# Kernel tuning notes

Hardware: AMD Instinct MI355X
Metric: run time of the kernel (lower is better)

Reference implementation:

```python
import jax, jax.numpy as jnp
import numpy as np

NUM_HEADS = 4
NUM_GROUPS = 32
EPS = 1e-6


def group_norm(x, gamma, beta):
    # x: [b, c, h, w]
    b, c, h, w = x.shape
    xg = x.reshape(b, NUM_GROUPS, c // NUM_GROUPS, h, w)
    mu = xg.mean(axis=(2, 3, 4), keepdims=True)
    var = xg.var(axis=(2, 3, 4), keepdims=True)
    xn = ((xg - mu) * jax.lax.rsqrt(var + EPS)).reshape(b, c, h, w)
    return xn * gamma[None, :, None, None] + beta[None, :, None, None]


def conv1x1(x, W, b):
    # 1x1 conv == per-pixel channel matmul. W: [out_c, in_c], b: [out_c]
    return jnp.einsum('bchw,oc->bohw', x, W) + b[None, :, None, None]


def setup_inputs() -> dict:
    key = jax.random.key(0)
    ks = jax.random.split(key, 8)
    c = 256
    b, h, w = 1, 64, 64
    s = 1.0 / np.sqrt(c)
    return {
        'x_kv': jax.random.normal(ks[0], (b, c, h, w), dtype=jnp.float32),
        'gn_gamma': jnp.ones((c,), dtype=jnp.float32),
        'gn_beta': jnp.zeros((c,), dtype=jnp.float32),
        'Wq': jax.random.normal(ks[1], (c, c), dtype=jnp.float32) * s,
        'bq': jnp.zeros((c,), dtype=jnp.float32),
        'Wk': jax.random.normal(ks[2], (c, c), dtype=jnp.float32) * s,
        'bk': jnp.zeros((c,), dtype=jnp.float32),
        'Wv': jax.random.normal(ks[3], (c, c), dtype=jnp.float32) * s,
        'bv': jnp.zeros((c,), dtype=jnp.float32),
        'Wp': jax.random.normal(ks[4], (c, c), dtype=jnp.float32) * s,
        'bp': jnp.zeros((c,), dtype=jnp.float32),
    }


def reference(x_kv, gn_gamma, gn_beta, Wq, bq, Wk, bk, Wv, bv, Wp, bp):
    b, c, h, w = x_kv.shape
    hd = c // NUM_HEADS
    n = h * w

    h_norm = group_norm(x_kv, gn_gamma, gn_beta)  # self-attn: same norm for q,k,v

    q = conv1x1(h_norm, Wq, bq).reshape(b, NUM_HEADS, hd, n).transpose(0, 1, 3, 2)  # [b,H,n,hd]
    k = conv1x1(h_norm, Wk, bk).reshape(b, NUM_HEADS, hd, n)                        # [b,H,hd,n]
    v = conv1x1(h_norm, Wv, bv).reshape(b, NUM_HEADS, hd, n).transpose(0, 1, 3, 2)  # [b,H,n,hd]

    scores = jnp.einsum('bhnd,bhdm->bhnm', q, k) * (hd ** -0.5)  # [b,H,n,n]
    attn = jax.nn.softmax(scores, axis=-1)
    out = jnp.einsum('bhnm,bhmd->bhnd', attn, v)  # [b,H,n,hd]

    # Faithful to torch: permute(0,2,1,3).contiguous().view(b,c,h,w)
    out = out.transpose(0, 2, 1, 3).reshape(b, c, h, w)
    return x_kv + conv1x1(out, Wp, bp)
```

## Files before the change

kernel.cpp:

```cpp
#include <hip/hip_runtime.h>
#include <hip/hip_bf16.h>

#define NPIX 4096
#define CCH  256
#define HD   64
#define GSIZE 32768

#define QSCALE 0.18033688f

typedef __bf16 bf16x8 __attribute__((ext_vector_type(8)));
typedef __bf16 bf16x4 __attribute__((ext_vector_type(4)));
typedef __bf16 bf16x2 __attribute__((ext_vector_type(2)));
typedef float  f32x4  __attribute__((ext_vector_type(4)));
typedef unsigned int uint32x4 __attribute__((ext_vector_type(4)));

#define XPITCH 264

#if __has_builtin(__builtin_amdgcn_exp2f)
#define EXP2(x) __builtin_amdgcn_exp2f(x)
#else
#define EXP2(x) __expf((x) * 0.6931471805599453f)
#endif


__device__ __forceinline__ unsigned pack_bf16x2(float lo, float hi)
{
    bf16x2 v;
    v[0] = (__bf16)lo;
    v[1] = (__bf16)hi;
    return __builtin_bit_cast(unsigned, v);
}

__global__ __launch_bounds__(256) void stats_wconv(
    const float* __restrict__ X,
    const float* __restrict__ Wq, const float* __restrict__ Wk,
    const float* __restrict__ Wv, const float* __restrict__ Wp,
    float* __restrict__ psum, float* __restrict__ pssq, __bf16* __restrict__ Wb)
{
    const int bid = blockIdx.x, t = threadIdx.x;
    if (bid < 256) {
        const float* base = X + bid * 4096;
        float sum = 0.f, ssq = 0.f;
        #pragma unroll
        for (int k = 0; k < 4; ++k) {
            float4 v = *(const float4*)(base + t * 4 + k * 1024);
            sum += v.x + v.y + v.z + v.w;
            ssq += v.x * v.x + v.y * v.y + v.z * v.z + v.w * v.w;
        }
        #pragma unroll
        for (int off = 1; off < 64; off <<= 1) {
            sum += __shfl_xor(sum, off);
            ssq += __shfl_xor(ssq, off);
        }
        __shared__ float red[2][4];
        const int wv = t >> 6;
        if ((t & 63) == 0) { red[0][wv] = sum; red[1][wv] = ssq; }
        __syncthreads();
        if (t == 0) {
            psum[bid] = red[0][0] + red[0][1] + red[0][2] + red[0][3];
            pssq[bid] = red[1][0] + red[1][1] + red[1][2] + red[1][3];
        }
    } else {
        const int j0 = (bid - 256) * 4096 + t * 16;
        const int m  = j0 >> 16;
        const float* W = (m == 0) ? Wq : (m == 1) ? Wk : (m == 2) ? Wv : Wp;
        const float sc = (m == 0) ? QSCALE : 1.f;
        const int off = j0 & 65535;
        #pragma unroll
        for (int k = 0; k < 4; ++k) {
            float4 v = *(const float4*)(W + off + k * 4);
            bf16x4 o;
            o[0] = (__bf16)(v.x * sc); o[1] = (__bf16)(v.y * sc);
            o[2] = (__bf16)(v.z * sc); o[3] = (__bf16)(v.w * sc);
            *(bf16x4*)(Wb + m * 65536 + off + k * 4) = o;
        }
    }
}

__global__ __launch_bounds__(256) void gn_qkv(
    const float* __restrict__ X, const float* __restrict__ gamma,
    const float* __restrict__ beta,
    const float* __restrict__ psum, const float* __restrict__ pssq,
    const __bf16* __restrict__ Wb,
    const float* __restrict__ bq, const float* __restrict__ bk,
    const float* __restrict__ bv,
    __bf16* __restrict__ Qb, __bf16* __restrict__ Kb, __bf16* __restrict__ Vb)
{
    __shared__ __bf16 tile[64 * XPITCH];
    __shared__ float al[256], bl[256];

    const int t = threadIdx.x, lane = t & 63, wave = t >> 6;
    const int l16 = lane & 15, quad = lane >> 4;
    const int p0 = blockIdx.x * 64;
    const int z = blockIdx.y >> 1, och = blockIdx.y & 1;

    {
        const int g = t >> 3;
        float s = 0.f, q = 0.f;
        #pragma unroll
        for (int j = 0; j < 8; ++j) { s += psum[g * 8 + j]; q += pssq[g * 8 + j]; }
        const float mu  = s * (1.f / GSIZE);
        const float var = q * (1.f / GSIZE) - mu * mu;
        const float a = gamma[t] * rsqrtf(var + 1e-6f);
        al[t] = a;
        bl[t] = beta[t] - mu * a;
    }
    __syncthreads();

    #pragma unroll 4
    for (int i = 0; i < 16; ++i) {
        const int c4 = wave * 64 + i * 4;
        f32x4 a4 = *(const f32x4*)(al + c4);
        f32x4 b4 = *(const f32x4*)(bl + c4);
        bf16x4 pk;
        pk[0] = (__bf16)(X[(c4 + 0) * NPIX + p0 + lane] * a4[0] + b4[0]);
        pk[1] = (__bf16)(X[(c4 + 1) * NPIX + p0 + lane] * a4[1] + b4[1]);
        pk[2] = (__bf16)(X[(c4 + 2) * NPIX + p0 + lane] * a4[2] + b4[2]);
        pk[3] = (__bf16)(X[(c4 + 3) * NPIX + p0 + lane] * a4[3] + b4[3]);
        *(bf16x4*)(tile + lane * XPITCH + c4) = pk;
    }
    __syncthreads();

    const int pw = wave * 16;
    bf16x8 xf[8];
    #pragma unroll
    for (int kc = 0; kc < 8; ++kc)
        xf[kc] = *(const bf16x8*)(tile + (pw + l16) * XPITCH + kc * 32 + quad * 8);

    const __bf16* Wz = Wb + z * 65536;
    const float* bias = (z == 0) ? bq : (z == 1) ? bk : bv;

    if (z < 2) {
        const float qs = (z == 0) ? QSCALE : 1.f;
        __bf16* dst = (z == 0) ? Qb : Kb;
        #pragma unroll
        for (int grp = 0; grp < 2; ++grp) {
            f32x4 acc[4] = {};
            #pragma unroll
            for (int kc = 0; kc < 8; ++kc) {
                #pragma unroll
                for (int u = 0; u < 4; ++u) {
                    bf16x8 wf = *(const bf16x8*)(Wz + (och * 128 + (grp * 4 + u) * 16 + l16) * CCH + kc * 32 + quad * 8);
                    acc[u] = __builtin_amdgcn_mfma_f32_16x16x32_bf16(wf, xf[kc], acc[u], 0, 0, 0);
                }
            }
            #pragma unroll
            for (int u = 0; u < 4; ++u) {
                const int ot = och * 8 + grp * 4 + u;
                f32x4 bz = *(const f32x4*)(bias + och * 128 + (grp * 4 + u) * 16 + quad * 4);
                bf16x4 o;
                o[0] = (__bf16)(acc[u][0] + bz[0] * qs);
                o[1] = (__bf16)(acc[u][1] + bz[1] * qs);
                o[2] = (__bf16)(acc[u][2] + bz[2] * qs);
                o[3] = (__bf16)(acc[u][3] + bz[3] * qs);
                const int head = ot >> 2, dloc = (ot & 3) * 16 + quad * 4;
                *(bf16x4*)(dst + head * (NPIX * HD) + (p0 + pw + l16) * HD + dloc) = o;
            }
        }
    } else {
        #pragma unroll
        for (int grp = 0; grp < 2; ++grp) {
            f32x4 acc[4] = {};
            #pragma unroll
            for (int kc = 0; kc < 8; ++kc) {
                #pragma unroll
                for (int u = 0; u < 4; ++u) {
                    bf16x8 wf = *(const bf16x8*)(Wz + (och * 128 + (grp * 4 + u) * 16 + l16) * CCH + kc * 32 + quad * 8);
                    acc[u] = __builtin_amdgcn_mfma_f32_16x16x32_bf16(xf[kc], wf, acc[u], 0, 0, 0);
                }
            }
            #pragma unroll
            for (int u = 0; u < 4; ++u) {
                const int oc = och * 128 + (grp * 4 + u) * 16 + l16;
                const float bz = bias[oc];
                bf16x4 o;
                o[0] = (__bf16)(acc[u][0] + bz); o[1] = (__bf16)(acc[u][1] + bz);
                o[2] = (__bf16)(acc[u][2] + bz); o[3] = (__bf16)(acc[u][3] + bz);
                *(bf16x4*)(Vb + oc * NPIX + p0 + pw + quad * 4) = o;
            }
        }
    }
}

__global__ __launch_bounds__(256, 1) void attn_mfma(
    const __bf16* __restrict__ Qb, const __bf16* __restrict__ Kb,
    const __bf16* __restrict__ Vb, __bf16* __restrict__ Sb)
{
    __shared__ __align__(16) float co[4 * 64 * 68];
    __shared__ float cl[4 * 64];

    const int t = threadIdx.x, lane = t & 63, wave = t >> 6;
    const int l16 = lane & 15, quad = lane >> 4;

    const int bid  = blockIdx.x;
    const int head = (bid & 7) >> 1;
    const int qt   = ((bid >> 3) << 1) | (bid & 1);
    const int p0   = qt * 64;

    const __bf16* Qh = Qb + head * (NPIX * HD);
    const __bf16* Kh = Kb + head * (NPIX * HD) + (wave * 32 + l16) * HD + quad * 8;
    const __bf16* Vh = Vb + head * (HD * NPIX) + l16 * NPIX + wave * 32 + quad * 8;

    bf16x8 qf[4][2];
    #pragma unroll
    for (int rt = 0; rt < 4; ++rt) {
        const __bf16* qp = Qh + (p0 + rt * 16 + l16) * HD + quad * 8;
        qf[rt][0] = *(const bf16x8*)(qp);
        qf[rt][1] = *(const bf16x8*)(qp + 32);
    }

    bf16x8 ones;
    #pragma unroll
    for (int j = 0; j < 8; ++j) ones[j] = (__bf16)1.0f;

    f32x4 l_acc[4] = {};
    f32x4 o_acc[4][4] = {};

    bf16x8 kA0, kA1, kA2, kA3, vA0, vA1, vA2, vA3;
    bf16x8 kB0, kB1, kB2, kB3, vB0, vB1, vB2, vB3;
    f32x4 sA0[4], sA1[4], sB0[4], sB1[4];
    bf16x8 bp[4];

    auto ldK = [&](int it, bf16x8& k0, bf16x8& k1, bf16x8& k2, bf16x8& k3) {
        const __bf16* kp = Kh + it * (128 * HD);
        k0 = *(const bf16x8*)(kp);
        k1 = *(const bf16x8*)(kp + 32);
        k2 = *(const bf16x8*)(kp + 16 * HD);
        k3 = *(const bf16x8*)(kp + 16 * HD + 32);
    };
    auto ldV = [&](int it, bf16x8& v0, bf16x8& v1, bf16x8& v2, bf16x8& v3) {
        const __bf16* vp = Vh + it * 128;
        v0 = *(const bf16x8*)(vp);
        v1 = *(const bf16x8*)(vp + 16 * NPIX);
        v2 = *(const bf16x8*)(vp + 32 * NPIX);
        v3 = *(const bf16x8*)(vp + 48 * NPIX);
    };
    auto qk = [&](bf16x8 k0, bf16x8 k1, bf16x8 k2, bf16x8 k3,
                  f32x4 (&s0)[4], f32x4 (&s1)[4]) {
        #pragma unroll
        for (int rt = 0; rt < 4; ++rt) {
            f32x4 z = {0.f, 0.f, 0.f, 0.f};
            s0[rt] = __builtin_amdgcn_mfma_f32_16x16x32_bf16(k0, qf[rt][0], z, 0, 0, 0);
            s0[rt] = __builtin_amdgcn_mfma_f32_16x16x32_bf16(k1, qf[rt][1], s0[rt], 0, 0, 0);
            s1[rt] = __builtin_amdgcn_mfma_f32_16x16x32_bf16(k2, qf[rt][0], z, 0, 0, 0);
            s1[rt] = __builtin_amdgcn_mfma_f32_16x16x32_bf16(k3, qf[rt][1], s1[rt], 0, 0, 0);
        }
    };
    auto exppack = [&](const f32x4 (&s0)[4], const f32x4 (&s1)[4]) {
        #pragma unroll
        for (int rt = 0; rt < 4; ++rt) {
            unsigned a0 = pack_bf16x2(EXP2(s0[rt][0]), EXP2(s0[rt][1]));
            unsigned a1 = pack_bf16x2(EXP2(s0[rt][2]), EXP2(s0[rt][3]));
            unsigned b0 = pack_bf16x2(EXP2(s1[rt][0]), EXP2(s1[rt][1]));
            unsigned b1 = pack_bf16x2(EXP2(s1[rt][2]), EXP2(s1[rt][3]));
            asm("v_permlane32_swap_b32 %0, %1" : "+v"(a0), "+v"(b0));
            asm("v_permlane32_swap_b32 %0, %1" : "+v"(a1), "+v"(b1));
            asm("v_permlane16_swap_b32 %0, %1" : "+v"(a0), "+v"(b0));
            asm("v_permlane16_swap_b32 %0, %1" : "+v"(a1), "+v"(b1));
            uint32x4 w;
            w[0] = a0; w[1] = a1; w[2] = b0; w[3] = b1;
            bp[rt] = __builtin_bit_cast(bf16x8, w);
        }
    };
    auto pv = [&](bf16x8 v0, bf16x8 v1, bf16x8 v2, bf16x8 v3) {
        #pragma unroll
        for (int rt = 0; rt < 4; ++rt) {
            l_acc[rt] = __builtin_amdgcn_mfma_f32_16x16x32_bf16(ones, bp[rt], l_acc[rt], 0, 0, 0);
            o_acc[0][rt] = __builtin_amdgcn_mfma_f32_16x16x32_bf16(v0, bp[rt], o_acc[0][rt], 0, 0, 0);
            o_acc[1][rt] = __builtin_amdgcn_mfma_f32_16x16x32_bf16(v1, bp[rt], o_acc[1][rt], 0, 0, 0);
            o_acc[2][rt] = __builtin_amdgcn_mfma_f32_16x16x32_bf16(v2, bp[rt], o_acc[2][rt], 0, 0, 0);
            o_acc[3][rt] = __builtin_amdgcn_mfma_f32_16x16x32_bf16(v3, bp[rt], o_acc[3][rt], 0, 0, 0);
        }
    };

    ldK(0, kA0, kA1, kA2, kA3);  ldV(0, vA0, vA1, vA2, vA3);
    ldK(1, kB0, kB1, kB2, kB3);  ldV(1, vB0, vB1, vB2, vB3);
    qk(kA0, kA1, kA2, kA3, sA0, sA1);

    #pragma unroll 1
    for (int it = 0; it < 32; it += 2) {
        const int n2 = (it + 2 < 32) ? it + 2 : 31;
        const int n3 = (it + 3 < 32) ? it + 3 : 31;

        qk(kB0, kB1, kB2, kB3, sB0, sB1);
        ldK(n2, kA0, kA1, kA2, kA3);
        exppack(sA0, sA1);
        pv(vA0, vA1, vA2, vA3);
        ldV(n2, vA0, vA1, vA2, vA3);
        exppack(sB0, sB1);
        qk(kA0, kA1, kA2, kA3, sA0, sA1);
        pv(vB0, vB1, vB2, vB3);
        ldK(n3, kB0, kB1, kB2, kB3);
        ldV(n3, vB0, vB1, vB2, vB3);
    }

    #pragma unroll
    for (int dt = 0; dt < 4; ++dt)
        #pragma unroll
        for (int rt = 0; rt < 4; ++rt)
            *(f32x4*)(co + wave * 4352 + (rt * 16 + l16) * 68 + dt * 16 + quad * 4) = o_acc[dt][rt];
    if (quad == 0) {
        #pragma unroll
        for (int rt = 0; rt < 4; ++rt)
            cl[wave * 64 + rt * 16 + l16] = l_acc[rt][0];
    }
    __syncthreads();

    {
        const int row = t >> 2, dc = (t & 3) * 16;
        const float l = cl[row] + cl[64 + row] + cl[128 + row] + cl[192 + row];
        const float inv = 1.f / l;
        f32x4 s[4];
        #pragma unroll
        for (int j = 0; j < 4; ++j) {
            s[j] = f32x4{0.f, 0.f, 0.f, 0.f};
            #pragma unroll
            for (int w = 0; w < 4; ++w)
                s[j] += *(const f32x4*)(co + w * 4352 + row * 68 + dc + j * 4);
        }
        bf16x8 o1, o2;
        #pragma unroll
        for (int j = 0; j < 4; ++j) {
            o1[j]     = (__bf16)(s[0][j] * inv);
            o1[j + 4] = (__bf16)(s[1][j] * inv);
            o2[j]     = (__bf16)(s[2][j] * inv);
            o2[j + 4] = (__bf16)(s[3][j] * inv);
        }
        __bf16* dst = Sb + (p0 + row) * CCH + head * HD + dc;
        *(bf16x8*)(dst)     = o1;
        *(bf16x8*)(dst + 8) = o2;
    }
}

__global__ __launch_bounds__(256) void gemm_proj(
    const __bf16* __restrict__ Sb, const __bf16* __restrict__ Wpb,
    const float* __restrict__ bias, const float* __restrict__ X,
    float* __restrict__ Out)
{
    __shared__ __bf16 Bs[32 * XPITCH];

    const int t = threadIdx.x, lane = t & 63, wave = t >> 6;
    const int l16 = lane & 15, quad = lane >> 4;
    const int p0  = blockIdx.x * 32;
    const int och = blockIdx.y;

    #pragma unroll
    for (int pg = 0; pg < 4; ++pg) {
        bf16x8 v = *(const bf16x8*)(Sb + t * NPIX + p0 + pg * 8);
        #pragma unroll
        for (int j = 0; j < 8; ++j)
            Bs[(pg * 8 + j) * XPITCH + t] = v[j];
    }
    __syncthreads();

    const int pixset = wave & 1, ocset = wave >> 1;
    bf16x8 af[8];
    #pragma unroll
    for (int kc = 0; kc < 8; ++kc)
        af[kc] = *(const bf16x8*)(Bs + (pixset * 16 + l16) * XPITCH + kc * 32 + quad * 8);

    #pragma unroll
    for (int u = 0; u < 4; ++u) {
        f32x4 acc = {};
        const int oc_t = och * 128 + ocset * 64 + u * 16;
        #pragma unroll
        for (int kc = 0; kc < 8; ++kc) {
            bf16x8 wf = *(const bf16x8*)(Wpb + (oc_t + l16) * CCH + kc * 32 + quad * 8);
            acc = __builtin_amdgcn_mfma_f32_16x16x32_bf16(af[kc], wf, acc, 0, 0, 0);
        }
        const int oc  = oc_t + l16;
        const int pix = p0 + pixset * 16 + quad * 4;
        const float bz = bias[oc];
        f32x4 r4 = *(const f32x4*)(X + oc * NPIX + pix);
        f32x4 y;
        y[0] = acc[0] + bz + r4[0];
        y[1] = acc[1] + bz + r4[1];
        y[2] = acc[2] + bz + r4[2];
        y[3] = acc[3] + bz + r4[3];
        *(f32x4*)(Out + oc * NPIX + pix) = y;
    }
}

extern "C" void kernel_launch(void* const* d_in, const int* in_sizes, int n_in,
                              void* d_out, int out_size, void* d_ws, size_t ws_size,
                              hipStream_t stream)
{
    const float* x     = (const float*)d_in[0];
    const float* gamma = (const float*)d_in[1];
    const float* beta  = (const float*)d_in[2];
    const float* Wq    = (const float*)d_in[3];
    const float* bq    = (const float*)d_in[4];
    const float* Wk    = (const float*)d_in[5];
    const float* bk    = (const float*)d_in[6];
    const float* Wv    = (const float*)d_in[7];
    const float* bv    = (const float*)d_in[8];
    const float* Wp    = (const float*)d_in[9];
    const float* bp    = (const float*)d_in[10];
    float* out = (float*)d_out;

    char* ws = (char*)d_ws;
    float*  psum = (float*)(ws);
    float*  pssq = (float*)(ws + 1024);
    __bf16* Wb   = (__bf16*)(ws + 65536);
    __bf16* Qb   = (__bf16*)(ws + (1 << 20));
    __bf16* Kb   = (__bf16*)(ws + (3 << 20));
    __bf16* Vb   = (__bf16*)(ws + (5 << 20));
    __bf16* Sb   = (__bf16*)(ws + (7 << 20));

    stats_wconv<<<320, 256, 0, stream>>>(x, Wq, Wk, Wv, Wp, psum, pssq, Wb);

    dim3 gq(64, 6);
    gn_qkv<<<gq, 256, 0, stream>>>(x, gamma, beta, psum, pssq, Wb,
                                   bq, bk, bv, Qb, Kb, Vb);

    attn_mfma<<<256, 256, 0, stream>>>(Qb, Kb, Vb, Sb);

    dim3 gp(128, 2);
    gemm_proj<<<gp, 256, 0, stream>>>(Sb, Wb + 3 * 65536, bp, x, out);
}
```

Measured before the change: 143.6 us.

## Restructure attention inner loop pipeline and fuse exp-pack with PV MMA

Replaces the software-pipelined loop, which computed QK one step ahead and prefetched K/V two iterations ahead, with a simpler schedule. Each half-iteration now loads only one step ahead, runs QK, then a fused exp/pack + PV MFMA step that no longer keeps the packed P tiles in a register array. This cuts live registers and the cross-iteration prologue, which may raise occupancy or let the compiler interleave better. The cost is a shorter prefetch distance, so memory latency is less hidden, and conditional loads are added at the tail.

```diff
diff --git a/kernel.cpp b/kernel.cpp
--- a/kernel.cpp
+++ b/kernel.cpp
@@ -216,11 +216,6 @@
     f32x4 l_acc[4] = {};
     f32x4 o_acc[4][4] = {};
 
-    bf16x8 kA0, kA1, kA2, kA3, vA0, vA1, vA2, vA3;
-    bf16x8 kB0, kB1, kB2, kB3, vB0, vB1, vB2, vB3;
-    f32x4 sA0[4], sA1[4], sB0[4], sB1[4];
-    bf16x8 bp[4];
-
     auto ldK = [&](int it, bf16x8& k0, bf16x8& k1, bf16x8& k2, bf16x8& k3) {
         const __bf16* kp = Kh + it * (128 * HD);
         k0 = *(const bf16x8*)(kp);
@@ -235,18 +230,22 @@
         v2 = *(const bf16x8*)(vp + 32 * NPIX);
         v3 = *(const bf16x8*)(vp + 48 * NPIX);
     };
+
     auto qk = [&](bf16x8 k0, bf16x8 k1, bf16x8 k2, bf16x8 k3,
                   f32x4 (&s0)[4], f32x4 (&s1)[4]) {
         #pragma unroll
         for (int rt = 0; rt < 4; ++rt) {
-            f32x4 z = {0.f, 0.f, 0.f, 0.f};
-            s0[rt] = __builtin_amdgcn_mfma_f32_16x16x32_bf16(k0, qf[rt][0], z, 0, 0, 0);
+            s0[rt] = f32x4{0.f, 0.f, 0.f, 0.f};
+            s1[rt] = f32x4{0.f, 0.f, 0.f, 0.f};
+            s0[rt] = __builtin_amdgcn_mfma_f32_16x16x32_bf16(k0, qf[rt][0], s0[rt], 0, 0, 0);
             s0[rt] = __builtin_amdgcn_mfma_f32_16x16x32_bf16(k1, qf[rt][1], s0[rt], 0, 0, 0);
-            s1[rt] = __builtin_amdgcn_mfma_f32_16x16x32_bf16(k2, qf[rt][0], z, 0, 0, 0);
+            s1[rt] = __builtin_amdgcn_mfma_f32_16x16x32_bf16(k2, qf[rt][0], s1[rt], 0, 0, 0);
             s1[rt] = __builtin_amdgcn_mfma_f32_16x16x32_bf16(k3, qf[rt][1], s1[rt], 0, 0, 0);
         }
     };
-    auto exppack = [&](const f32x4 (&s0)[4], const f32x4 (&s1)[4]) {
+
+    auto pvx = [&](const f32x4 (&s0)[4], const f32x4 (&s1)[4],
+                   bf16x8 v0, bf16x8 v1, bf16x8 v2, bf16x8 v3) {
         #pragma unroll
         for (int rt = 0; rt < 4; ++rt) {
             unsigned a0 = pack_bf16x2(EXP2(s0[rt][0]), EXP2(s0[rt][1]));
@@ -259,39 +258,32 @@
             asm("v_permlane16_swap_b32 %0, %1" : "+v"(a1), "+v"(b1));
             uint32x4 w;
             w[0] = a0; w[1] = a1; w[2] = b0; w[3] = b1;
-            bp[rt] = __builtin_bit_cast(bf16x8, w);
+            const bf16x8 bp = __builtin_bit_cast(bf16x8, w);
+            l_acc[rt] = __builtin_amdgcn_mfma_f32_16x16x32_bf16(ones, bp, l_acc[rt], 0, 0, 0);
+            o_acc[0][rt] = __builtin_amdgcn_mfma_f32_16x16x32_bf16(v0, bp, o_acc[0][rt], 0, 0, 0);
+            o_acc[1][rt] = __builtin_amdgcn_mfma_f32_16x16x32_bf16(v1, bp, o_acc[1][rt], 0, 0, 0);
+            o_acc[2][rt] = __builtin_amdgcn_mfma_f32_16x16x32_bf16(v2, bp, o_acc[2][rt], 0, 0, 0);
+            o_acc[3][rt] = __builtin_amdgcn_mfma_f32_16x16x32_bf16(v3, bp, o_acc[3][rt], 0, 0, 0);
         }
     };
-    auto pv = [&](bf16x8 v0, bf16x8 v1, bf16x8 v2, bf16x8 v3) {
-        #pragma unroll
-        for (int rt = 0; rt < 4; ++rt) {
-            l_acc[rt] = __builtin_amdgcn_mfma_f32_16x16x32_bf16(ones, bp[rt], l_acc[rt], 0, 0, 0);
-            o_acc[0][rt] = __builtin_amdgcn_mfma_f32_16x16x32_bf16(v0, bp[rt], o_acc[0][rt], 0, 0, 0);
-            o_acc[1][rt] = __builtin_amdgcn_mfma_f32_16x16x32_bf16(v1, bp[rt], o_acc[1][rt], 0, 0, 0);
-            o_acc[2][rt] = __builtin_amdgcn_mfma_f32_16x16x32_bf16(v2, bp[rt], o_acc[2][rt], 0, 0, 0);
-            o_acc[3][rt] = __builtin_amdgcn_mfma_f32_16x16x32_bf16(v3, bp[rt], o_acc[3][rt], 0, 0, 0);
-        }
-    };
-
-    ldK(0, kA0, kA1, kA2, kA3);  ldV(0, vA0, vA1, vA2, vA3);
-    ldK(1, kB0, kB1, kB2, kB3);  ldV(1, vB0, vB1, vB2, vB3);
-    qk(kA0, kA1, kA2, kA3, sA0, sA1);
+
+    bf16x8 kA0, kA1, kA2, kA3, vA0, vA1, vA2, vA3;
+    bf16x8 kB0, kB1, kB2, kB3, vB0, vB1, vB2, vB3;
+    f32x4 sA0[4], sA1[4], sB0[4], sB1[4];
+
+    ldK(0, kA0, kA1, kA2, kA3);
+    ldV(0, vA0, vA1, vA2, vA3);
 
     #pragma unroll 1
     for (int it = 0; it < 32; it += 2) {
-        const int n2 = (it + 2 < 32) ? it + 2 : 31;
-        const int n3 = (it + 3 < 32) ? it + 3 : 31;
-
+        ldK(it + 1, kB0, kB1, kB2, kB3);
+        qk(kA0, kA1, kA2, kA3, sA0, sA1);
+        ldV(it + 1, vB0, vB1, vB2, vB3);
+        pvx(sA0, sA1, vA0, vA1, vA2, vA3);
+        if (it + 2 < 32) ldK(it + 2, kA0, kA1, kA2, kA3);
         qk(kB0, kB1, kB2, kB3, sB0, sB1);
-        ldK(n2, kA0, kA1, kA2, kA3);
-        exppack(sA0, sA1);
-        pv(vA0, vA1, vA2, vA3);
-        ldV(n2, vA0, vA1, vA2, vA3);
-        exppack(sB0, sB1);
-        qk(kA0, kA1, kA2, kA3, sA0, sA1);
-        pv(vB0, vB1, vB2, vB3);
-        ldK(n3, kB0, kB1, kB2, kB3);
-        ldV(n3, vB0, vB1, vB2, vB3);
+        if (it + 2 < 32) ldV(it + 2, vA0, vA1, vA2, vA3);
+        pvx(sB0, sB1, vB0, vB1, vB2, vB3);
     }
 
     #pragma unroll
```

New measurement: 141.6 us. Within noise of the previous version (-1.3%).
